# Performance work log

Hardware: AMD Instinct MI355X
Metric: run time of the kernel (lower is better)

The kernel has to match this reference:

```python
import jax, jax.numpy as jnp
import numpy as np

DEPTH = 4
CHUNK = 16


def tp(a, b):
    """Graded tensor (outer) product on flattened levels: (...,m)x(...,n)->(...,m*n)."""
    return jnp.einsum('...i,...j->...ij', a, b).reshape(*a.shape[:-1], a.shape[-1] * b.shape[-1])


def ta_mul(a, b):
    """Truncated tensor-algebra product of two group-like elements (implicit level-0 == 1).
    a, b: lists of levels 1..D, level k flattened to C**k."""
    out = []
    for k in range(len(a)):
        t = a[k] + b[k]
        for i in range(k):
            t = t + tp(a[i], b[k - 1 - i])
        out.append(t)
    return out


def ta_mulz(a, b):
    """Product when both elements have level-0 == 0."""
    out = []
    for k in range(len(a)):
        t = jnp.zeros_like(a[k])
        for i in range(k):
            t = t + tp(a[i], b[k - 1 - i])
        out.append(t)
    return out


def ta_exp(a):
    """exp of a level-0-free element, truncated at DEPTH; returns levels 1..D (level-0 == 1 implicit)."""
    out = list(a)
    p = a
    fact = 1.0
    for m in range(2, len(a) + 1):
        p = ta_mulz(a, p)
        fact *= m
        out = [o + q / fact for o, q in zip(out, p)]
    return out


def ta_log(s):
    """Truncated log of group-like element g = 1 + s; input s = levels 1..D of g."""
    out = list(s)
    p = s
    sign = 1.0
    for m in range(2, len(s) + 1):
        p = ta_mulz(s, p)
        sign = -sign
        out = [o + (sign / m) * q for o, q in zip(out, p)]
    return out


def bch(a, b):
    """BCH merge: log(exp(a) (x) exp(b)) in the truncated algebra."""
    return ta_log(ta_mul(ta_exp(a), ta_exp(b)))


def exp_l1(d):
    """exp of a pure level-1 element d (shape (...,C)): level k = d^(x)k / k!."""
    levels = [d]
    cur = d
    fact = 1.0
    for k in range(2, DEPTH + 1):
        cur = tp(cur, d)
        fact *= k
        levels.append(cur / fact)
    return levels


def chunk_signatures(inc):
    """inc: (B, N, L, C) per-chunk increments -> signature levels [(B,N,C), (B,N,C^2), ...]
    via Chen: sig = exp(d_1) (x) ... (x) exp(d_L)."""
    carry0 = tuple(exp_l1(inc[:, :, 0]))
    xs = jnp.moveaxis(inc[:, :, 1:], 2, 0)  # (L-1, B, N, C)
    def step(carry, d):
        return tuple(ta_mul(list(carry), exp_l1(d))), None
    carry, _ = jax.lax.scan(step, carry0, xs)
    return list(carry)


def hillis_steele(levels):
    """Inclusive associative scan over chunk dim (axis=1) with BCH merge.
    bch(0, b) == b exactly, so zero-padding handles the boundary."""
    N = levels[0].shape[1]
    pref = levels
    d = 1
    while d < N:
        shifted = [jnp.concatenate([jnp.zeros_like(l[:, :d]), l[:, :-d]], axis=1) for l in pref]
        pref = bch(shifted, pref)
        d *= 2
    return pref


def _forward(x, W1, b1, W2, b2):
    B, T, Cin = x.shape
    t = jnp.linspace(0.0, 1.0, T, dtype=x.dtype)
    path = jnp.concatenate([x, jnp.broadcast_to(t[None, :, None], (B, T, 1)).astype(x.dtype)], axis=-1)
    C = Cin + 1
    # basepoint=True: path starts at 0, so increments are diff of [0; path]
    inc = jnp.diff(path, axis=1, prepend=jnp.zeros((B, 1, C), x.dtype))
    N = T // CHUNK
    inc = inc.reshape(B, N, CHUNK, C)
    sig = chunk_signatures(inc)          # levels 1..D, (B,N,C^k)
    logl = ta_log(sig)                   # truncated log-signature per chunk
    pref = hillis_steele(logl)           # inclusive BCH prefix scan
    flat = jnp.concatenate(pref, axis=-1)  # (B, N, mem_dim)
    pooled = flat.mean(axis=1)           # readout_pool == 'mean'
    h = jnp.maximum(pooled @ W1 + b1, 0.0)
    return h @ W2 + b2


def setup_inputs() -> dict:
    key = jax.random.key(0)
    k0, k1, k2 = jax.random.split(key, 3)
    B, T, Cin = 8, 2048, 7
    mem_dim, H, out_dim = 4680, 256, 1
    x = jax.random.normal(k0, (B, T, Cin), dtype=jnp.float32)
    W1 = jax.random.normal(k1, (mem_dim, H), dtype=jnp.float32) * (1.0 / np.sqrt(mem_dim))
    b1 = jnp.zeros((H,), jnp.float32)
    W2 = jax.random.normal(k2, (H, out_dim), dtype=jnp.float32) * (1.0 / np.sqrt(H))
    b2 = jnp.zeros((out_dim,), jnp.float32)
    return {"x": x, "W1": W1, "b1": b1, "W2": W2, "b2": b2}


def reference(x, W1, b1, W2, b2):
    return _forward(x, W1, b1, W2, b2)
```

## Files before the change

kernel.cpp:

```cpp
#include <hip/hip_runtime.h>


#define MEM   4680
#define HG    64
#define TLEN  2048
#define P3OFF 72
#define P4OFF 648
#define SIGSZ 5256

__device__ __forceinline__ void load_padded(float* dst, const float* __restrict__ src, int tid) {
    if (tid < 72) dst[tid] = src[tid];
    for (int e = tid; e < 512; e += 256) dst[P3OFF + (e >> 3) * 9 + (e & 7)] = src[72 + e];
    for (int e = tid; e < 4096; e += 256) dst[P4OFF + (e >> 3) * 9 + (e & 7)] = src[584 + e];
}

__device__ __forceinline__ void load_inc32(const float* __restrict__ x, int b, int h,
                                           float* sInc, int tid) {
    int s = tid >> 3, c = tid & 7;
    int t = h * 32 + s;
    float v;
    if (c < 7) {
        float cur  = x[(b * TLEN + t) * 7 + c];
        float prev = (t > 0) ? x[(b * TLEN + t - 1) * 7 + c] : 0.f;
        v = cur - prev;
    } else v = (t > 0) ? (1.f / 2047.f) : 0.f;
    sInc[tid] = v;
}

#define CHUNK_RECUR(dch)                                                            \
    float p1a = 0.f, l2a = 0.f, l3a = 0.f, p1b = 0.f, l2b = 0.f, l3b = 0.f;         \
    float Sa[8], Sb[8];                                                             \
    _Pragma("unroll")                                                               \
    for (int l = 0; l < 8; l++) { Sa[l] = 0.f; Sb[l] = 0.f; }                       \
    _Pragma("unroll")                                                               \
    for (int t = 0; t < 16; t++) {                                                  \
        const float* dr = (dch) + t * 8;                                            \
        float di1 = dr[i1], di2 = dr[i2], dj = dr[j1], dk = dr[k1];                 \
        float ga = l3a + dk * (l2a * 0.5f + dj * (p1a * (1.f/6.f) + di1 * (1.f/24.f))); \
        float gb = l3b + dk * (l2b * 0.5f + dj * (p1b * (1.f/6.f) + di2 * (1.f/24.f))); \
        _Pragma("unroll")                                                           \
        for (int l = 0; l < 8; l++) { float dv = dr[l]; Sa[l] += ga * dv; Sb[l] += gb * dv; } \
        l3a += dk * (l2a + dj * (p1a * 0.5f + di1 * (1.f/6.f)));                    \
        l3b += dk * (l2b + dj * (p1b * 0.5f + di2 * (1.f/6.f)));                    \
        l2a += (p1a + di1 * 0.5f) * dj;                                             \
        l2b += (p1b + di2 * 0.5f) * dj;                                             \
        p1a += di1; p1b += di2;                                                     \
    }

__device__ __forceinline__ void chunk_step_first(const float* dch, float* sA, int tid) {
    const int i1 = tid >> 6, j1 = (tid >> 3) & 7, k1 = tid & 7;
    const int row1 = tid >> 3, row2 = row1 + 32;
    const int pos2 = tid + 256, i2 = pos2 >> 6;
    CHUNK_RECUR(dch)
#pragma unroll
    for (int l = 0; l < 8; l++) { sA[P4OFF + tid * 9 + l] = Sa[l]; sA[P4OFF + pos2 * 9 + l] = Sb[l]; }
    sA[P3OFF + row1 * 9 + k1] = l3a;
    sA[P3OFF + row2 * 9 + k1] = l3b;
    if (k1 == 0) { sA[8 + row1] = l2a; sA[8 + row2] = l2b; }
    if ((tid & 63) == 0) { sA[i1] = p1a; sA[i2] = p1b; }
    __syncthreads();
}

__device__ __forceinline__ void chunk_step(const float* dch, float* sA, float* U, int tid) {
    float* loc3 = U;
    float* loc2 = U + 576;
    float* loc1 = U + 640;
    const int i1 = tid >> 6, j1 = (tid >> 3) & 7, k1 = tid & 7;
    const int row1 = tid >> 3, row2 = row1 + 32;
    const int jk = tid & 63;
    const int pos2 = tid + 256, i2 = pos2 >> 6;
    CHUNK_RECUR(dch)
    loc3[row1 * 9 + k1] = l3a;
    loc3[row2 * 9 + k1] = l3b;
    if (k1 == 0) { loc2[row1] = l2a; loc2[row2] = l2b; }
    if (jk == 0) { loc1[i1] = p1a; loc1[i2] = p1b; }
    __syncthreads();
    float a1 = sA[i1], a2 = sA[8 + row1], a3 = sA[P3OFF + row1 * 9 + k1];
    float c1_ = sA[i2], c2_ = sA[8 + row2], c3_ = sA[P3OFF + row2 * 9 + k1];
    const float* l3p = &loc3[jk * 9];
    const float* l2p = &loc2[k1 * 8];
    float n4a[8], n4b[8];
#pragma unroll
    for (int l = 0; l < 8; l++) {
        float v3 = l3p[l], v2 = l2p[l], v1 = loc1[l];
        n4a[l] = sA[P4OFF + tid * 9 + l]  + Sa[l] + a1 * v3 + a2 * v2 + a3 * v1;
        n4b[l] = sA[P4OFF + pos2 * 9 + l] + Sb[l] + c1_ * v3 + c2_ * v2 + c3_ * v1;
    }
    float n3a = a3 + l3a + a1 * loc2[jk] + a2 * loc1[k1];
    float n3b = c3_ + l3b + c1_ * loc2[jk] + c2_ * loc1[k1];
    float n2v = 0.f, n1v = 0.f;
    if (tid < 64) n2v = sA[8 + tid] + loc2[tid] + sA[tid >> 3] * loc1[tid & 7];
    if (tid < 8)  n1v = sA[tid] + loc1[tid];
    __syncthreads();
#pragma unroll
    for (int l = 0; l < 8; l++) { sA[P4OFF + tid * 9 + l] = n4a[l]; sA[P4OFF + pos2 * 9 + l] = n4b[l]; }
    sA[P3OFF + row1 * 9 + k1] = n3a;
    sA[P3OFF + row2 * 9 + k1] = n3b;
    if (tid < 64) sA[8 + tid] = n2v;
    if (tid < 8)  sA[tid] = n1v;
    __syncthreads();
}

__global__ __launch_bounds__(256) void sig_half_kernel(const float* __restrict__ x,
                                                       float* __restrict__ T) {
    int blk = blockIdx.x;
    int b = blk >> 6, h = blk & 63;
    int tid = threadIdx.x;
    __shared__ __attribute__((aligned(16))) float sInc[256];
    __shared__ __attribute__((aligned(16))) float sA[SIGSZ];
    __shared__ __attribute__((aligned(16))) float U[648];

    load_inc32(x, b, h, sInc, tid);
    __syncthreads();
    chunk_step_first(&sInc[0], sA, tid);
    chunk_step(&sInc[128], sA, U, tid);

    size_t base = (size_t)blk * MEM;
    for (int m = tid; m < MEM; m += 256) {
        float v;
        if (m < 72) v = sA[m];
        else if (m < 584) { int e = m - 72;  v = sA[P3OFF + (e >> 3) * 9 + (e & 7)]; }
        else              { int e = m - 584; v = sA[P4OFF + (e >> 3) * 9 + (e & 7)]; }
        T[base + m] = v;
    }
}

__global__ __launch_bounds__(256) void scan_fused_kernel(const float* __restrict__ T,
                                                         float* __restrict__ P) {
    int bx = blockIdx.x;
    int b = bx >> 4, s = bx & 15;
    int tid = threadIdx.x;

    __shared__ float st1[HG][8];
    __shared__ float st2[HG][64];
    __shared__ float st3[HG][32];
    __shared__ float sp1[HG][8];
    __shared__ float sp2[HG][64];
    __shared__ float sp3[HG][32];

    int bBase = b * HG;
    for (int m = tid; m < HG * 8; m += 256) {
        int g = m >> 3, i = m & 7;
        st1[g][i] = T[(size_t)(bBase + g) * MEM + i];
    }
    for (int m = tid; m < HG * 64; m += 256) {
        int g = m >> 6, e = m & 63;
        st2[g][e] = T[(size_t)(bBase + g) * MEM + 8 + e];
    }
    for (int m = tid; m < HG * 32; m += 256) {
        int g = m >> 5, e = m & 31;
        st3[g][e] = T[(size_t)(bBase + g) * MEM + 72 + s * 32 + e];
    }
    __syncthreads();

    if (tid < 64) {
        int i = tid >> 3, k = tid & 7;
        float p1acc = 0.f, p2acc = 0.f;
        for (int g = 0; g < HG; g++) {
            sp2[g][tid] = p2acc;
            if (k == 0) sp1[g][i] = p1acc;
            if (s == 0) {
                size_t prow = (size_t)(bBase + g) * MEM;
                P[prow + 8 + tid] = p2acc;
                if (k == 0) P[prow + i] = p1acc;
            }
            p2acc += st2[g][tid] + p1acc * st1[g][k];
            p1acc += st1[g][i];
        }
    }
    __syncthreads();
    if (tid < 32) {
        int ijk = s * 32 + tid;
        int i = ijk >> 6, jk = ijk & 63, ij = ijk >> 3, k = ijk & 7;
        float acc3 = 0.f;
        for (int g = 0; g < HG; g++) {
            sp3[g][tid] = acc3;
            P[(size_t)(bBase + g) * MEM + 72 + ijk] = acc3;
            acc3 += st3[g][tid] + sp1[g][i] * st2[g][jk] + sp2[g][ij] * st1[g][k];
        }
    }
    __syncthreads();
    {
        int m = s * 256 + tid;
        int i = m >> 9, jkl = m & 511, ij = m >> 6, kl = m & 63, l = m & 7;
        int p3loc = tid >> 3;
        float acc4 = 0.f;
#pragma unroll 4
        for (int g = 0; g < HG; g++) {
            size_t row = (size_t)(bBase + g) * MEM;
            P[row + 584 + m] = acc4;
            acc4 += T[row + 584 + m]
                  + sp1[g][i] * T[row + 72 + jkl]
                  + sp2[g][ij] * st2[g][kl]
                  + sp3[g][p3loc] * st1[g][l];
        }
    }
}

__global__ __launch_bounds__(256) void apply_log_kernel(const float* __restrict__ x,
                                                        const float* __restrict__ P,
                                                        float* __restrict__ partial) {
    int blk = blockIdx.x;
    int b = blk >> 6, h = blk & 63;
    int tid = threadIdx.x;

    __shared__ __attribute__((aligned(16))) float sInc[256];
    __shared__ __attribute__((aligned(16))) float sA[SIGSZ];
    __shared__ __attribute__((aligned(16))) float sP[SIGSZ];
    __shared__ __attribute__((aligned(16))) float U[648];
    __shared__ __attribute__((aligned(16))) float sR[648];
    __shared__ __attribute__((aligned(16))) float sQ23[576];

    load_inc32(x, b, h, sInc, tid);
    load_padded(sP, P + (size_t)blk * MEM, tid);
    __syncthreads();

    const int i1 = tid >> 6, j1 = (tid >> 3) & 7, k1 = tid & 7;
    const int row1 = tid >> 3, row2 = row1 + 32;
    const int jk = tid & 63;
    const int pos2 = tid + 256, i2 = pos2 >> 6;

    float pool4a[8], pool4b[8];
#pragma unroll
    for (int l = 0; l < 8; l++) { pool4a[l] = 0.f; pool4b[l] = 0.f; }
    float pool3a = 0.f, pool3b = 0.f, pool2 = 0.f, pool1 = 0.f;

    for (int c = 0; c < 2; c++) {
        if (c == 0) chunk_step_first(&sInc[0], sA, tid);
        else        chunk_step(&sInc[128], sA, U, tid);

        float a1 = sP[i1], a2 = sP[8 + row1], a3 = sP[P3OFF + row1 * 9 + k1];
        float c1_ = sP[i2], c2_ = sP[8 + row2], c3_ = sP[P3OFF + row2 * 9 + k1];
        const float* b3p = &sA[P3OFF + jk * 9];
        const float* b2p = &sA[8 + k1 * 8];
        float R4a[8], R4b[8];
#pragma unroll
        for (int l = 0; l < 8; l++) {
            float v3 = b3p[l], v2 = b2p[l], v1 = sA[l];
            R4a[l] = sP[P4OFF + tid * 9 + l]  + sA[P4OFF + tid * 9 + l]  + a1 * v3 + a2 * v2 + a3 * v1;
            R4b[l] = sP[P4OFF + pos2 * 9 + l] + sA[P4OFF + pos2 * 9 + l] + c1_ * v3 + c2_ * v2 + c3_ * v1;
        }
        float R3a = a3 + sA[P3OFF + row1 * 9 + k1] + a1 * sA[8 + jk] + a2 * sA[k1];
        float R3b = c3_ + sA[P3OFF + row2 * 9 + k1] + c1_ * sA[8 + jk] + c2_ * sA[k1];
        float R2v = 0.f, R1v = 0.f;
        if (tid < 64) R2v = sP[8 + tid] + sA[8 + tid] + sP[tid >> 3] * sA[tid & 7];
        if (tid < 8)  R1v = sP[tid] + sA[tid];

        sR[P3OFF + row1 * 9 + k1] = R3a;
        sR[P3OFF + row2 * 9 + k1] = R3b;
        if (tid < 64) sR[8 + tid] = R2v;
        if (tid < 8)  sR[tid] = R1v;
        __syncthreads();

        float q23a = sR[i1] * sR[8 + jk] + sR[8 + row1] * sR[k1];
        float q23b = sR[i2] * sR[8 + jk] + sR[8 + row2] * sR[k1];
        sQ23[row1 * 9 + k1] = q23a;
        sQ23[row2 * 9 + k1] = q23b;
        __syncthreads();

        {
            float s1ia = sR[i1], s1ib = sR[i2], s1j = sR[j1], s1k = sR[k1];
            float s2ija = sR[8 + row1], s2ijb = sR[8 + row2];
            const float* r3p = &sR[P3OFF + jk * 9];
            const float* r2p = &sR[8 + k1 * 8];
            const float* q23p = &sQ23[jk * 9];
#pragma unroll
            for (int l = 0; l < 8; l++) {
                float s1l = sR[l];
                float p22 = s1k * s1l;
                float p24a = s1ia * r3p[l] + s2ija * r2p[l] + R3a * s1l;
                float p24b = s1ib * r3p[l] + s2ijb * r2p[l] + R3b * s1l;
                float p34a = s1ia * q23p[l] + s2ija * p22;
                float p34b = s1ib * q23p[l] + s2ijb * p22;
                float p44a = s1ia * s1j * p22;
                float p44b = s1ib * s1j * p22;
                pool4a[l] += R4a[l] - 0.5f * p24a + (1.f/3.f) * p34a - 0.25f * p44a;
                pool4b[l] += R4b[l] - 0.5f * p24b + (1.f/3.f) * p34b - 0.25f * p44b;
            }
            pool3a += R3a - 0.5f * q23a + (1.f/3.f) * s1ia * s1j * s1k;
            pool3b += R3b - 0.5f * q23b + (1.f/3.f) * s1ib * s1j * s1k;
            if (tid < 64) pool2 += R2v - 0.5f * sR[tid >> 3] * sR[tid & 7];
            if (tid < 8)  pool1 += R1v;
        }
        __syncthreads();
    }

    {
        float* pb = partial + (size_t)blk * MEM;
        float4* d1 = (float4*)(pb + 584 + tid * 8);
        d1[0] = make_float4(pool4a[0], pool4a[1], pool4a[2], pool4a[3]);
        d1[1] = make_float4(pool4a[4], pool4a[5], pool4a[6], pool4a[7]);
        float4* d2 = (float4*)(pb + 584 + pos2 * 8);
        d2[0] = make_float4(pool4b[0], pool4b[1], pool4b[2], pool4b[3]);
        d2[1] = make_float4(pool4b[4], pool4b[5], pool4b[6], pool4b[7]);
        pb[72 + tid] = pool3a;
        pb[72 + pos2] = pool3b;
        if (tid < 64) pb[8 + tid] = pool2;
        if (tid < 8)  pb[tid] = pool1;
    }
}

__global__ __launch_bounds__(256) void gemv1_kernel(const float* __restrict__ partial,
                                                    const float* __restrict__ W1,
                                                    float* __restrict__ hpart) {
    int kc = blockIdx.x;
    int tid = threadIdx.x;
    int k0 = kc * 32;
    __shared__ float sp[8][32];
    {
        int b = tid >> 5, k = tid & 31;
        float sum = 0.f;
        if (k0 + k < MEM) {
#pragma unroll 4
            for (int g = 0; g < HG; g++)
                sum += partial[(size_t)(b * HG + g) * MEM + k0 + k];
        }
        sp[b][k] = sum * (1.f / 128.f);
    }
    __syncthreads();
    float acc[8];
#pragma unroll
    for (int b = 0; b < 8; b++) acc[b] = 0.f;
    int kend = (k0 + 32 < MEM) ? 32 : (MEM - k0);
    for (int k = 0; k < kend; k++) {
        float wv = W1[(size_t)(k0 + k) * 256 + tid];
#pragma unroll
        for (int b = 0; b < 8; b++) acc[b] += sp[b][k] * wv;
    }
#pragma unroll
    for (int b = 0; b < 8; b++) hpart[(size_t)kc * 2048 + b * 256 + tid] = acc[b];
}

__global__ __launch_bounds__(256) void final_kernel(const float* __restrict__ hpart,
                                                    const float* __restrict__ b1,
                                                    const float* __restrict__ W2,
                                                    const float* __restrict__ b2,
                                                    float* __restrict__ outp) {
    int b = blockIdx.x;
    int tid = threadIdx.x;
    float v = 0.f;
    for (int kc = 0; kc < 147; kc++) v += hpart[(size_t)kc * 2048 + b * 256 + tid];
    v += b1[tid];
    v = fmaxf(v, 0.f) * W2[tid];
    __shared__ float sRed[256];
    sRed[tid] = v;
    __syncthreads();
    for (int s = 128; s > 0; s >>= 1) {
        if (tid < s) sRed[tid] += sRed[tid + s];
        __syncthreads();
    }
    if (tid == 0) outp[b] = sRed[0] + b2[0];
}

extern "C" void kernel_launch(void* const* d_in, const int* in_sizes, int n_in,
                              void* d_out, int out_size, void* d_ws, size_t ws_size,
                              hipStream_t stream) {
    const float* x  = (const float*)d_in[0];
    const float* W1 = (const float*)d_in[1];
    const float* b1 = (const float*)d_in[2];
    const float* W2 = (const float*)d_in[3];
    const float* b2 = (const float*)d_in[4];
    float* out = (float*)d_out;

    float* ws = (float*)d_ws;
    float* T       = ws;
    float* P       = T + (size_t)512 * MEM;
    float* partial = P + (size_t)512 * MEM;
    float* hpart   = partial + (size_t)512 * MEM;

    sig_half_kernel<<<512, 256, 0, stream>>>(x, T);
    scan_fused_kernel<<<128, 256, 0, stream>>>(T, P);
    apply_log_kernel<<<512, 256, 0, stream>>>(x, P, partial);
    gemv1_kernel<<<147, 256, 0, stream>>>(partial, W1, hpart);
    final_kernel<<<8, 256, 0, stream>>>(hpart, b1, W2, b2, out);
}
```

Before: 141.6 us.

## Coarsen signature totals to 64-step groups and halve the prefix scan length

```diff
diff --git a/kernel.cpp b/kernel.cpp
--- a/kernel.cpp
+++ b/kernel.cpp
@@ -2,7 +2,7 @@
 
 
 #define MEM   4680
-#define HG    64
+#define NG    32
 #define TLEN  2048
 #define P3OFF 72
 #define P4OFF 648
@@ -14,20 +14,22 @@
     for (int e = tid; e < 4096; e += 256) dst[P4OFF + (e >> 3) * 9 + (e & 7)] = src[584 + e];
 }
 
-__device__ __forceinline__ void load_inc32(const float* __restrict__ x, int b, int h,
+__device__ __forceinline__ void load_inc64(const float* __restrict__ x, int b, int g,
                                            float* sInc, int tid) {
-    int s = tid >> 3, c = tid & 7;
-    int t = h * 32 + s;
-    float v;
-    if (c < 7) {
-        float cur  = x[(b * TLEN + t) * 7 + c];
-        float prev = (t > 0) ? x[(b * TLEN + t - 1) * 7 + c] : 0.f;
-        v = cur - prev;
-    } else v = (t > 0) ? (1.f / 2047.f) : 0.f;
-    sInc[tid] = v;
-}
-
-#define CHUNK_RECUR(dch)                                                            \
+    for (int e = tid; e < 512; e += 256) {
+        int s = e >> 3, c = e & 7;
+        int t = g * 64 + s;
+        float v;
+        if (c < 7) {
+            float cur  = x[(b * TLEN + t) * 7 + c];
+            float prev = (t > 0) ? x[(b * TLEN + t - 1) * 7 + c] : 0.f;
+            v = cur - prev;
+        } else v = (t > 0) ? (1.f / 2047.f) : 0.f;
+        sInc[e] = v;
+    }
+}
+
+#define CHUNK_RECUR2(dch)                                                           \
     float p1a = 0.f, l2a = 0.f, l3a = 0.f, p1b = 0.f, l2b = 0.f, l3b = 0.f;         \
     float Sa[8], Sb[8];                                                             \
     _Pragma("unroll")                                                               \
@@ -51,7 +53,7 @@
     const int i1 = tid >> 6, j1 = (tid >> 3) & 7, k1 = tid & 7;
     const int row1 = tid >> 3, row2 = row1 + 32;
     const int pos2 = tid + 256, i2 = pos2 >> 6;
-    CHUNK_RECUR(dch)
+    CHUNK_RECUR2(dch)
 #pragma unroll
     for (int l = 0; l < 8; l++) { sA[P4OFF + tid * 9 + l] = Sa[l]; sA[P4OFF + pos2 * 9 + l] = Sb[l]; }
     sA[P3OFF + row1 * 9 + k1] = l3a;
@@ -59,6 +61,7 @@
     if (k1 == 0) { sA[8 + row1] = l2a; sA[8 + row2] = l2b; }
     if ((tid & 63) == 0) { sA[i1] = p1a; sA[i2] = p1b; }
     __syncthreads();
+    (void)j1;
 }
 
 __device__ __forceinline__ void chunk_step(const float* dch, float* sA, float* U, int tid) {
@@ -69,7 +72,7 @@
     const int row1 = tid >> 3, row2 = row1 + 32;
     const int jk = tid & 63;
     const int pos2 = tid + 256, i2 = pos2 >> 6;
-    CHUNK_RECUR(dch)
+    CHUNK_RECUR2(dch)
     loc3[row1 * 9 + k1] = l3a;
     loc3[row2 * 9 + k1] = l3b;
     if (k1 == 0) { loc2[row1] = l2a; loc2[row2] = l2b; }
@@ -99,21 +102,24 @@
     if (tid < 64) sA[8 + tid] = n2v;
     if (tid < 8)  sA[tid] = n1v;
     __syncthreads();
-}
-
-__global__ __launch_bounds__(256) void sig_half_kernel(const float* __restrict__ x,
-                                                       float* __restrict__ T) {
+    (void)j1;
+}
+
+__global__ __launch_bounds__(256) void sig_totals_kernel(const float* __restrict__ x,
+                                                         float* __restrict__ T) {
     int blk = blockIdx.x;
-    int b = blk >> 6, h = blk & 63;
-    int tid = threadIdx.x;
-    __shared__ __attribute__((aligned(16))) float sInc[256];
+    int b = blk >> 5, g = blk & 31;
+    int tid = threadIdx.x;
+    __shared__ __attribute__((aligned(16))) float sInc[512];
     __shared__ __attribute__((aligned(16))) float sA[SIGSZ];
     __shared__ __attribute__((aligned(16))) float U[648];
 
-    load_inc32(x, b, h, sInc, tid);
+    load_inc64(x, b, g, sInc, tid);
     __syncthreads();
     chunk_step_first(&sInc[0], sA, tid);
     chunk_step(&sInc[128], sA, U, tid);
+    chunk_step(&sInc[256], sA, U, tid);
+    chunk_step(&sInc[384], sA, U, tid);
 
     size_t base = (size_t)blk * MEM;
     for (int m = tid; m < MEM; m += 256) {
@@ -131,23 +137,23 @@
     int b = bx >> 4, s = bx & 15;
     int tid = threadIdx.x;
 
-    __shared__ float st1[HG][8];
-    __shared__ float st2[HG][64];
-    __shared__ float st3[HG][32];
-    __shared__ float sp1[HG][8];
-    __shared__ float sp2[HG][64];
-    __shared__ float sp3[HG][32];
-
-    int bBase = b * HG;
-    for (int m = tid; m < HG * 8; m += 256) {
-        int g = m >> 3, i = m & 7;
+    __shared__ float st1[NG][8];
+    __shared__ float st2[NG][64];
+    __shared__ float st3[NG][32];
+    __shared__ float sp1[NG][8];
+    __shared__ float sp2[NG][64];
+    __shared__ float sp3[NG][32];
+
+    int bBase = b * NG;
+    {
+        int g = tid >> 3, i = tid & 7;
         st1[g][i] = T[(size_t)(bBase + g) * MEM + i];
     }
-    for (int m = tid; m < HG * 64; m += 256) {
+    for (int m = tid; m < NG * 64; m += 256) {
         int g = m >> 6, e = m & 63;
         st2[g][e] = T[(size_t)(bBase + g) * MEM + 8 + e];
     }
-    for (int m = tid; m < HG * 32; m += 256) {
+    for (int m = tid; m < NG * 32; m += 256) {
         int g = m >> 5, e = m & 31;
         st3[g][e] = T[(size_t)(bBase + g) * MEM + 72 + s * 32 + e];
     }
@@ -156,7 +162,7 @@
     if (tid < 64) {
         int i = tid >> 3, k = tid & 7;
         float p1acc = 0.f, p2acc = 0.f;
-        for (int g = 0; g < HG; g++) {
+        for (int g = 0; g < NG; g++) {
             sp2[g][tid] = p2acc;
             if (k == 0) sp1[g][i] = p1acc;
             if (s == 0) {
@@ -173,7 +179,7 @@
         int ijk = s * 32 + tid;
         int i = ijk >> 6, jk = ijk & 63, ij = ijk >> 3, k = ijk & 7;
         float acc3 = 0.f;
-        for (int g = 0; g < HG; g++) {
+        for (int g = 0; g < NG; g++) {
             sp3[g][tid] = acc3;
             P[(size_t)(bBase + g) * MEM + 72 + ijk] = acc3;
             acc3 += st3[g][tid] + sp1[g][i] * st2[g][jk] + sp2[g][ij] * st1[g][k];
@@ -186,7 +192,7 @@
         int p3loc = tid >> 3;
         float acc4 = 0.f;
 #pragma unroll 4
-        for (int g = 0; g < HG; g++) {
+        for (int g = 0; g < NG; g++) {
             size_t row = (size_t)(bBase + g) * MEM;
             P[row + 584 + m] = acc4;
             acc4 += T[row + 584 + m]
@@ -197,22 +203,22 @@
     }
 }
 
-__global__ __launch_bounds__(256) void apply_log_kernel(const float* __restrict__ x,
-                                                        const float* __restrict__ P,
-                                                        float* __restrict__ partial) {
+__global__ __launch_bounds__(256) void apply_log_pool_kernel(const float* __restrict__ x,
+                                                             const float* __restrict__ P,
+                                                             float* __restrict__ partial) {
     int blk = blockIdx.x;
-    int b = blk >> 6, h = blk & 63;
-    int tid = threadIdx.x;
-
-    __shared__ __attribute__((aligned(16))) float sInc[256];
+    int b = blk >> 6, rest = blk & 63, g = rest >> 1, h = rest & 1;
+    int tid = threadIdx.x;
+
+    __shared__ __attribute__((aligned(16))) float sInc[512];
     __shared__ __attribute__((aligned(16))) float sA[SIGSZ];
     __shared__ __attribute__((aligned(16))) float sP[SIGSZ];
     __shared__ __attribute__((aligned(16))) float U[648];
     __shared__ __attribute__((aligned(16))) float sR[648];
     __shared__ __attribute__((aligned(16))) float sQ23[576];
 
-    load_inc32(x, b, h, sInc, tid);
-    load_padded(sP, P + (size_t)blk * MEM, tid);
+    load_inc64(x, b, g, sInc, tid);
+    load_padded(sP, P + (size_t)(b * NG + g) * MEM, tid);
     __syncthreads();
 
     const int i1 = tid >> 6, j1 = (tid >> 3) & 7, k1 = tid & 7;
@@ -225,9 +231,17 @@
     for (int l = 0; l < 8; l++) { pool4a[l] = 0.f; pool4b[l] = 0.f; }
     float pool3a = 0.f, pool3b = 0.f, pool2 = 0.f, pool1 = 0.f;
 
-    for (int c = 0; c < 2; c++) {
-        if (c == 0) chunk_step_first(&sInc[0], sA, tid);
-        else        chunk_step(&sInc[128], sA, U, tid);
+    chunk_step_first(&sInc[0], sA, tid);
+    if (h == 1) {
+        chunk_step(&sInc[128], sA, U, tid);
+        chunk_step(&sInc[256], sA, U, tid);
+    }
+
+    for (int cc = 0; cc < 2; cc++) {
+        if (!(h == 0 && cc == 0)) {
+            if (cc == 1) chunk_step(&sInc[(h * 2 + 1) * 128], sA, U, tid);
+        }
+        if (h == 1 && cc == 1) {  }
 
         float a1 = sP[i1], a2 = sP[8 + row1], a3 = sP[P3OFF + row1 * 9 + k1];
         float c1_ = sP[i2], c2_ = sP[8 + row2], c3_ = sP[P3OFF + row2 * 9 + k1];
@@ -312,8 +326,8 @@
         float sum = 0.f;
         if (k0 + k < MEM) {
 #pragma unroll 4
-            for (int g = 0; g < HG; g++)
-                sum += partial[(size_t)(b * HG + g) * MEM + k0 + k];
+            for (int r = 0; r < 64; r++)
+                sum += partial[(size_t)(b * 64 + r) * MEM + k0 + k];
         }
         sp[b][k] = sum * (1.f / 128.f);
     }
@@ -364,13 +378,13 @@
 
     float* ws = (float*)d_ws;
     float* T       = ws;
-    float* P       = T + (size_t)512 * MEM;
-    float* partial = P + (size_t)512 * MEM;
+    float* P       = T + (size_t)256 * MEM;
+    float* partial = P + (size_t)256 * MEM;
     float* hpart   = partial + (size_t)512 * MEM;
 
-    sig_half_kernel<<<512, 256, 0, stream>>>(x, T);
+    sig_totals_kernel<<<256, 256, 0, stream>>>(x, T);
     scan_fused_kernel<<<128, 256, 0, stream>>>(T, P);
-    apply_log_kernel<<<512, 256, 0, stream>>>(x, P, partial);
+    apply_log_pool_kernel<<<512, 256, 0, stream>>>(x, P, partial);
     gemv1_kernel<<<147, 256, 0, stream>>>(partial, W1, hpart);
     final_kernel<<<8, 256, 0, stream>>>(hpart, b1, W2, b2, out);
 }
```

Measured after the change: 142.4 us. About the same (+0.6%).
